# Performance work log

Measured on AMD Instinct MI355X. Metric: run time of the kernel, lower is better.

Reference implementation:

```python
import jax, jax.numpy as jnp
import numpy as np

B, T, IN, H, OUT = 2048, 4096, 1, 8, 1


def setup_inputs() -> dict:
    key = jax.random.key(0)
    ks = jax.random.split(key, 11)
    s_in = 1.0 / np.sqrt(H)  # torch nn.LSTM/Linear init scale (uniform +-1/sqrt(H))
    u = lambda k, shape, s: jax.random.uniform(k, shape, jnp.float32, -s, s)
    return {
        "input_seq": jax.random.normal(ks[0], (B, T, IN), jnp.float32),
        # layer 0 (input_size=IN)
        "W_ih0": u(ks[1], (4 * H, IN), s_in),
        "W_hh0": u(ks[2], (4 * H, H), s_in),
        "b_ih0": u(ks[3], (4 * H,), s_in),
        "b_hh0": u(ks[4], (4 * H,), s_in),
        # layer 1 (input_size=H)
        "W_ih1": u(ks[5], (4 * H, H), s_in),
        "W_hh1": u(ks[6], (4 * H, H), s_in),
        "b_ih1": u(ks[7], (4 * H,), s_in),
        "b_hh1": u(ks[8], (4 * H,), s_in),
        # output projection
        "W_lin": u(ks[9], (OUT, H), s_in),
        "b_lin": u(ks[10], (OUT,), s_in),
    }


def _lstm_layer(x_tbi, W_ih, W_hh, b_ih, b_hh):
    """x_tbi: [T, B, in] -> hidden sequence [T, B, H]. PyTorch gate order i,f,g,o."""
    h_dim = W_hh.shape[1]
    # precompute input contribution for all timesteps (hoisted out of the scan)
    xg = jnp.einsum('tbi,gi->tbg', x_tbi, W_ih) + (b_ih + b_hh)  # [T, B, 4H]
    bsz = x_tbi.shape[1]
    h0 = jnp.zeros((bsz, h_dim), x_tbi.dtype)
    c0 = jnp.zeros((bsz, h_dim), x_tbi.dtype)

    def step(carry, xg_t):
        h, c = carry
        gates = xg_t + h @ W_hh.T  # [B, 4H]
        i, f, g, o = jnp.split(gates, 4, axis=-1)
        i = jax.nn.sigmoid(i)
        f = jax.nn.sigmoid(f)
        g = jnp.tanh(g)
        o = jax.nn.sigmoid(o)
        c = f * c + i * g
        h = o * jnp.tanh(c)
        return (h, c), h

    _, hs = jax.lax.scan(step, (h0, c0), xg)
    return hs  # [T, B, H]


def reference(input_seq, W_ih0, W_hh0, b_ih0, b_hh0,
              W_ih1, W_hh1, b_ih1, b_hh1, W_lin, b_lin):
    x = jnp.transpose(input_seq, (1, 0, 2))  # [T, B, IN] (batch_first -> time-major)
    h1 = _lstm_layer(x, W_ih0, W_hh0, b_ih0, b_hh0)   # [T, B, H]
    h2 = _lstm_layer(h1, W_ih1, W_hh1, b_ih1, b_hh1)  # [T, B, H]
    out = jnp.transpose(h2, (1, 0, 2))                # [B, T, H]
    pred = out @ W_lin.T + b_lin                      # [B, T, OUT]
    return pred
```

## Files before the change

### kernel.cpp

```cpp
#include <hip/hip_runtime.h>


constexpr int Bsz = 2048;
constexpr int Tsz = 4096;

typedef float v2f __attribute__((ext_vector_type(2)));

__device__ __forceinline__ void pk_fma(v2f& acc, v2f a, v2f b) {
    asm("v_pk_fma_f32 %0, %1, %2, %0" : "+v"(acc) : "v"(a), "v"(b));
}

template <int CTRL>
__device__ __forceinline__ float dpp(float v) {
    return __int_as_float(
        __builtin_amdgcn_mov_dpp(__float_as_int(v), CTRL, 0xF, 0xF, true));
}

__device__ __forceinline__ float swz16(float v) {
    return __int_as_float(
        __builtin_amdgcn_ds_swizzle(__float_as_int(v), 0x401F));
}

__global__ void __launch_bounds__(256) lstm2_dpp(
    const float* __restrict__ x,
    const float* __restrict__ Wih0,
    const float* __restrict__ Whh0,
    const float* __restrict__ bih0,
    const float* __restrict__ bhh0,
    const float* __restrict__ Wih1,
    const float* __restrict__ Whh1,
    const float* __restrict__ bih1,
    const float* __restrict__ bhh1,
    const float* __restrict__ Wlin,
    const float* __restrict__ blin,
    float* __restrict__ out)
{
    const int tid  = threadIdx.x;
    const int l32  = tid & 31;
    const int p    = l32 & 1;
    const int j    = (l32 >> 1) & 7;
    const int L    = (l32 >> 4) & 1;
    const bool pb  = (p != 0);
    const int seq  = blockIdx.x * 8 + (tid >> 5);

    const int rA = p * 16 + j;
    const int rB = p * 16 + 8 + j;

    const float NL2E  = -1.4426950408889634f;
    const float N2L2E = -2.8853900817779268f;
    const float wsA = pb ? N2L2E : NL2E;
    const float wsB = NL2E;
    const float sA  = pb ? 2.0f : 1.0f;
    const float oA  = pb ? -1.0f : 0.0f;

    const float* __restrict__ Whh = L ? Whh1 : Whh0;
    const float* __restrict__ bih = L ? bih1 : bih0;
    const float* __restrict__ bhh = L ? bhh1 : bhh0;

    v2f wp1A[4], wp1B[4], wp2A[4], wp2B[4];
#pragma unroll
    for (int q = 0; q < 4; ++q) {
        const int kx = j ^ (2 * q);
        const int ky = j ^ (2 * q + 1);
        wp1A[q] = v2f{Whh[rA * 8 + kx] * wsA, Whh[rA * 8 + ky] * wsA};
        wp1B[q] = v2f{Whh[rB * 8 + kx] * wsB, Whh[rB * 8 + ky] * wsB};
        if (L) {
            wp2A[q] = v2f{Wlin[kx], Wlin[ky]};
            wp2B[q] = v2f{0.0f, 0.0f};
        } else {
            wp2A[q] = v2f{Wih1[rA * 8 + kx] * wsA, Wih1[rA * 8 + ky] * wsA};
            wp2B[q] = v2f{Wih1[rB * 8 + kx] * wsB, Wih1[rB * 8 + ky] * wsB};
        }
    }
    const float wxA   = L ? 0.0f : Wih0[rA] * wsA;
    const float wxB   = L ? 0.0f : Wih0[rB] * wsB;
    const float biasA = (bih[rA] + bhh[rA]) * wsA;
    const float biasB = (bih[rB] + bhh[rB]) * wsB;
    const float b2A   = L ? blin[0] : 0.0f;
    const float mL    = L ? 1.0f : 0.0f;
    const float keep  = 1.0f - mL;

    const float* __restrict__ xp = x + (size_t)seq * Tsz;
    float* __restrict__ op       = out + (size_t)seq * Tsz;
    const bool storeLane = (l32 == 16);

    v2f hp[4];
#pragma unroll
    for (int q = 0; q < 4; ++q) hp[q] = v2f{0.0f, 0.0f};
    float c = 0.0f, h = 0.0f;
    float recvA = 0.0f, recvB = 0.0f;

    float xn1 = xp[0];
    float xn2 = xp[1];

    auto body = [&](int t) {
        const float xt = xn1;
        xn1 = xn2;
        int ti = t + 2; ti = (ti < Tsz) ? ti : (Tsz - 1);
        xn2 = xp[ti];

        v2f a1A = v2f{fmaf(wxA, xt, biasA), 0.0f};
        v2f a1B = v2f{fmaf(wxB, xt, biasB), 0.0f};
        v2f a2A = v2f{b2A, 0.0f};
        v2f a2B = v2f{0.0f, 0.0f};
#pragma unroll
        for (int q = 0; q < 4; ++q) {
            pk_fma(a1A, wp1A[q], hp[q]);
            pk_fma(a1B, wp1B[q], hp[q]);
            pk_fma(a2A, wp2A[q], hp[q]);
            pk_fma(a2B, wp2B[q], hp[q]);
        }
        const float d1A = a1A.x + a1A.y;
        const float d1B = a1B.x + a1B.y;
        const float d2A = a2A.x + a2A.y;
        const float d2B = a2B.x + a2B.y;

        if (t >= 3 && storeLane) op[t - 3] = d2A;

        const float rAo = recvA, rBo = recvB;
        recvA = swz16(d2A);
        recvB = swz16(d2B);

        const float zA = fmaf(mL, rAo, d1A);
        const float zB = fmaf(mL, rBo, d1B);

        float aA = fmaf(sA,
                        __builtin_amdgcn_rcpf(1.0f + __builtin_amdgcn_exp2f(zA)),
                        oA);
        float aB = __builtin_amdgcn_rcpf(1.0f + __builtin_amdgcn_exp2f(zB));
        const float xA = dpp<0xB1>(aA);
        const float xB = dpp<0xB1>(aB);
        const float gi = pb ? xA : aA;
        const float gg = pb ? aA : xA;
        const float gf = pb ? xB : aB;
        const float go = pb ? aB : xB;
        c = fmaf(gf, c, gi * gg);
        const float e  = __builtin_amdgcn_exp2f(c * N2L2E);
        const float th = fmaf(2.0f, __builtin_amdgcn_rcpf(1.0f + e), -1.0f);
        h = go * th;

        const float g0  = h;
        const float g2  = dpp<0x4E>(h);
        const float mB  = dpp<0x141>(h);
        const float g4  = dpp<0x1B>(mB);
        const float g6  = dpp<0xB1>(mB);
        const float mC  = dpp<0x140>(h);
        const float g12 = dpp<0x1B>(mC);
        const float g14 = dpp<0xB1>(mC);
        const float g8  = dpp<0x141>(mC);
        const float g10 = dpp<0x4E>(g8);
        hp[0] = v2f{g0, g2};
        hp[1] = v2f{g4, g6};
        hp[2] = v2f{g8, g10};
        hp[3] = v2f{g12, g14};
    };

    body(0);
    h *= keep; c *= keep;
#pragma unroll
    for (int q = 0; q < 4; ++q) { hp[q].x *= keep; hp[q].y *= keep; }
    body(1);
    h *= keep; c *= keep;
#pragma unroll
    for (int q = 0; q < 4; ++q) { hp[q].x *= keep; hp[q].y *= keep; }

    for (int t = 2; t <= Tsz + 2; ++t) body(t);
}

extern "C" void kernel_launch(void* const* d_in, const int* in_sizes, int n_in,
                              void* d_out, int out_size, void* d_ws, size_t ws_size,
                              hipStream_t stream) {
    const float* x    = (const float*)d_in[0];
    const float* Wih0 = (const float*)d_in[1];
    const float* Whh0 = (const float*)d_in[2];
    const float* bih0 = (const float*)d_in[3];
    const float* bhh0 = (const float*)d_in[4];
    const float* Wih1 = (const float*)d_in[5];
    const float* Whh1 = (const float*)d_in[6];
    const float* bih1 = (const float*)d_in[7];
    const float* bhh1 = (const float*)d_in[8];
    const float* Wlin = (const float*)d_in[9];
    const float* blin = (const float*)d_in[10];
    float* out = (float*)d_out;

    dim3 grid(Bsz / 8);
    dim3 block(256);
    hipLaunchKernelGGL(lstm2_dpp, grid, block, 0, stream,
                       x, Wih0, Whh0, bih0, bhh0,
                       Wih1, Whh1, bih1, bhh1, Wlin, blin, out);
}
```

Before: 1.004 ms.

## Map one LSTM sequence per 64-lane wave with one gate row per lane

Each sequence now occupies a full 64-lane wave instead of 32 lanes, so every lane computes a single gate row (4 gates × 8 units × 2 layers) rather than two. This halves the per-lane FMA and transcendental work on the serial recurrence path. Gate exchange now uses quad-broadcast DPP, the hidden-state gather uses ds_swizzle, and the layer-to-layer handoff uses ds_bpermute, which adds LDS-unit latency to each step. The grid doubles to 4 sequences per block, and launch bounds request 2 blocks per CU.

After: 948.5 us. 1.06x faster.

```diff
diff --git a/kernel.cpp b/kernel.cpp
--- a/kernel.cpp
+++ b/kernel.cpp
@@ -16,12 +16,18 @@
         __builtin_amdgcn_mov_dpp(__float_as_int(v), CTRL, 0xF, 0xF, true));
 }
 
-__device__ __forceinline__ float swz16(float v) {
+template <int XORM>
+__device__ __forceinline__ float swz(float v) {
     return __int_as_float(
-        __builtin_amdgcn_ds_swizzle(__float_as_int(v), 0x401F));
+        __builtin_amdgcn_ds_swizzle(__float_as_int(v), (XORM << 10) | 0x1f));
 }
 
-__global__ void __launch_bounds__(256) lstm2_dpp(
+__device__ __forceinline__ float bperm(int addr, float v) {
+    return __int_as_float(
+        __builtin_amdgcn_ds_bpermute(addr, __float_as_int(v)));
+}
+
+__global__ void __launch_bounds__(256, 2) lstm2_q64(
     const float* __restrict__ x,
     const float* __restrict__ Wih0,
     const float* __restrict__ Whh0,
@@ -36,59 +42,49 @@
     float* __restrict__ out)
 {
     const int tid  = threadIdx.x;
-    const int l32  = tid & 31;
-    const int p    = l32 & 1;
-    const int j    = (l32 >> 1) & 7;
-    const int L    = (l32 >> 4) & 1;
-    const bool pb  = (p != 0);
-    const int seq  = blockIdx.x * 8 + (tid >> 5);
+    const int lane = tid & 63;
+    const int g    = lane & 3;
+    const int j    = (lane >> 2) & 7;
+    const int L    = (lane >> 5) & 1;
+    const int seq  = blockIdx.x * 4 + (tid >> 6);
 
-    const int rA = p * 16 + j;
-    const int rB = p * 16 + 8 + j;
+    const int r = g * 8 + j;
 
     const float NL2E  = -1.4426950408889634f;
     const float N2L2E = -2.8853900817779268f;
-    const float wsA = pb ? N2L2E : NL2E;
-    const float wsB = NL2E;
-    const float sA  = pb ? 2.0f : 1.0f;
-    const float oA  = pb ? -1.0f : 0.0f;
+    const bool  isG   = (g == 2);
+    const float ws    = isG ? N2L2E : NL2E;
+    const float sA    = isG ? 2.0f : 1.0f;
+    const float oA    = isG ? -1.0f : 0.0f;
 
     const float* __restrict__ Whh = L ? Whh1 : Whh0;
     const float* __restrict__ bih = L ? bih1 : bih0;
     const float* __restrict__ bhh = L ? bhh1 : bhh0;
 
-    v2f wp1A[4], wp1B[4], wp2A[4], wp2B[4];
+    v2f wp1[4], wp2[4];
 #pragma unroll
     for (int q = 0; q < 4; ++q) {
         const int kx = j ^ (2 * q);
         const int ky = j ^ (2 * q + 1);
-        wp1A[q] = v2f{Whh[rA * 8 + kx] * wsA, Whh[rA * 8 + ky] * wsA};
-        wp1B[q] = v2f{Whh[rB * 8 + kx] * wsB, Whh[rB * 8 + ky] * wsB};
-        if (L) {
-            wp2A[q] = v2f{Wlin[kx], Wlin[ky]};
-            wp2B[q] = v2f{0.0f, 0.0f};
-        } else {
-            wp2A[q] = v2f{Wih1[rA * 8 + kx] * wsA, Wih1[rA * 8 + ky] * wsA};
-            wp2B[q] = v2f{Wih1[rB * 8 + kx] * wsB, Wih1[rB * 8 + ky] * wsB};
-        }
+        wp1[q] = v2f{Whh[r * 8 + kx] * ws, Whh[r * 8 + ky] * ws};
+        wp2[q] = L ? v2f{Wlin[kx], Wlin[ky]}
+                   : v2f{Wih1[r * 8 + kx] * ws, Wih1[r * 8 + ky] * ws};
     }
-    const float wxA   = L ? 0.0f : Wih0[rA] * wsA;
-    const float wxB   = L ? 0.0f : Wih0[rB] * wsB;
-    const float biasA = (bih[rA] + bhh[rA]) * wsA;
-    const float biasB = (bih[rB] + bhh[rB]) * wsB;
-    const float b2A   = L ? blin[0] : 0.0f;
-    const float mL    = L ? 1.0f : 0.0f;
-    const float keep  = 1.0f - mL;
+    const float bias = (bih[r] + bhh[r]) * ws;
+    const float wx   = L ? 0.0f : Wih0[r] * ws;
+    const float b2   = L ? blin[0] : 0.0f;
+    const float mL   = L ? 1.0f : 0.0f;
+    const float keep = 1.0f - mL;
+    const int  xaddr = (lane ^ 32) * 4;
 
     const float* __restrict__ xp = x + (size_t)seq * Tsz;
     float* __restrict__ op       = out + (size_t)seq * Tsz;
-    const bool storeLane = (l32 == 16);
+    const bool storeLane = (lane == 32);
 
     v2f hp[4];
 #pragma unroll
     for (int q = 0; q < 4; ++q) hp[q] = v2f{0.0f, 0.0f};
-    float c = 0.0f, h = 0.0f;
-    float recvA = 0.0f, recvB = 0.0f;
+    float c = 0.0f, h = 0.0f, recv = 0.0f;
 
     float xn1 = xp[0];
     float xn2 = xp[1];
@@ -99,60 +95,47 @@
         int ti = t + 2; ti = (ti < Tsz) ? ti : (Tsz - 1);
         xn2 = xp[ti];
 
-        v2f a1A = v2f{fmaf(wxA, xt, biasA), 0.0f};
-        v2f a1B = v2f{fmaf(wxB, xt, biasB), 0.0f};
-        v2f a2A = v2f{b2A, 0.0f};
-        v2f a2B = v2f{0.0f, 0.0f};
+        v2f a1 = v2f{fmaf(wx, xt, bias), 0.0f};
+        v2f a2 = v2f{b2, 0.0f};
 #pragma unroll
         for (int q = 0; q < 4; ++q) {
-            pk_fma(a1A, wp1A[q], hp[q]);
-            pk_fma(a1B, wp1B[q], hp[q]);
-            pk_fma(a2A, wp2A[q], hp[q]);
-            pk_fma(a2B, wp2B[q], hp[q]);
+            pk_fma(a1, wp1[q], hp[q]);
+            pk_fma(a2, wp2[q], hp[q]);
         }
-        const float d1A = a1A.x + a1A.y;
-        const float d1B = a1B.x + a1B.y;
-        const float d2A = a2A.x + a2A.y;
-        const float d2B = a2B.x + a2B.y;
+        const float d1 = a1.x + a1.y;
+        const float d2 = a2.x + a2.y;
 
-        if (t >= 3 && storeLane) op[t - 3] = d2A;
+        if (t >= 3 && storeLane) op[t - 3] = d2;
 
-        const float rAo = recvA, rBo = recvB;
-        recvA = swz16(d2A);
-        recvB = swz16(d2B);
+        const float rOld = recv;
+        recv = bperm(xaddr, d2);
 
-        const float zA = fmaf(mL, rAo, d1A);
-        const float zB = fmaf(mL, rBo, d1B);
-
-        float aA = fmaf(sA,
-                        __builtin_amdgcn_rcpf(1.0f + __builtin_amdgcn_exp2f(zA)),
-                        oA);
-        float aB = __builtin_amdgcn_rcpf(1.0f + __builtin_amdgcn_exp2f(zB));
-        const float xA = dpp<0xB1>(aA);
-        const float xB = dpp<0xB1>(aB);
-        const float gi = pb ? xA : aA;
-        const float gg = pb ? aA : xA;
-        const float gf = pb ? xB : aB;
-        const float go = pb ? aB : xB;
-        c = fmaf(gf, c, gi * gg);
+        const float z = fmaf(mL, rOld, d1);
+        float a = fmaf(sA,
+                       __builtin_amdgcn_rcpf(1.0f + __builtin_amdgcn_exp2f(z)),
+                       oA);
+        const float gi = dpp<0x00>(a);
+        const float gf = dpp<0x55>(a);
+        const float gG = dpp<0xAA>(a);
+        const float go = dpp<0xFF>(a);
+        c = fmaf(gf, c, gi * gG);
         const float e  = __builtin_amdgcn_exp2f(c * N2L2E);
         const float th = fmaf(2.0f, __builtin_amdgcn_rcpf(1.0f + e), -1.0f);
         h = go * th;
 
-        const float g0  = h;
-        const float g2  = dpp<0x4E>(h);
-        const float mB  = dpp<0x141>(h);
-        const float g4  = dpp<0x1B>(mB);
-        const float g6  = dpp<0xB1>(mB);
-        const float mC  = dpp<0x140>(h);
-        const float g12 = dpp<0x1B>(mC);
-        const float g14 = dpp<0xB1>(mC);
-        const float g8  = dpp<0x141>(mC);
-        const float g10 = dpp<0x4E>(g8);
-        hp[0] = v2f{g0, g2};
-        hp[1] = v2f{g4, g6};
-        hp[2] = v2f{g8, g10};
-        hp[3] = v2f{g12, g14};
+        const float m7  = dpp<0x141>(h);
+        const float h1_ = dpp<0x1B>(m7);
+        const float m15 = dpp<0x140>(h);
+        const float h2_ = dpp<0x141>(m15);
+        const float h3_ = dpp<0x1B>(m15);
+        const float h4_ = swz<16>(h);
+        const float h5_ = swz<20>(h);
+        const float h6_ = swz<24>(h);
+        const float h7_ = swz<28>(h);
+        hp[0] = v2f{h,   h1_};
+        hp[1] = v2f{h2_, h3_};
+        hp[2] = v2f{h4_, h5_};
+        hp[3] = v2f{h6_, h7_};
     };
 
     body(0);
@@ -183,9 +166,9 @@
     const float* blin = (const float*)d_in[10];
     float* out = (float*)d_out;
 
-    dim3 grid(Bsz / 8);
+    dim3 grid(Bsz / 4);
     dim3 block(256);
-    hipLaunchKernelGGL(lstm2_dpp, grid, block, 0, stream,
+    hipLaunchKernelGGL(lstm2_q64, grid, block, 0, stream,
                        x, Wih0, Whh0, bih0, bhh0,
                        Wih1, Whh1, bih1, bhh1, Wlin, blin, out);
 }
```
